# Kernel tuning notes

Hardware: AMD Instinct MI355X
Metric: run time of the kernel (lower is better)

## Reference

```python
import jax, jax.numpy as jnp
import numpy as np

N_NODES = 50000
N_EDGES = 800000
IN_FEATS = 512
NUM_HEADS = 4
OUT_FEATS = 64
NEG_SLOPE = 0.2


def setup_inputs() -> dict:
    key = jax.random.key(0)
    k1, k2, k3, k4, k5, k6 = jax.random.split(key, 6)
    feat = jax.random.normal(k1, (N_NODES, IN_FEATS), dtype=jnp.float32)
    W = jax.random.normal(k2, (IN_FEATS, NUM_HEADS * OUT_FEATS), dtype=jnp.float32) * (1.0 / np.sqrt(IN_FEATS))
    attn_l = jax.random.normal(k3, (NUM_HEADS, OUT_FEATS), dtype=jnp.float32) * (1.0 / np.sqrt(OUT_FEATS))
    attn_r = jax.random.normal(k4, (NUM_HEADS, OUT_FEATS), dtype=jnp.float32) * (1.0 / np.sqrt(OUT_FEATS))
    src = jax.random.randint(k5, (N_EDGES,), 0, N_NODES, dtype=jnp.int32)
    dst = jax.random.randint(k6, (N_EDGES,), 0, N_NODES, dtype=jnp.int32)
    return {"feat": feat, "W": W, "attn_l": attn_l, "attn_r": attn_r, "src": src, "dst": dst}


def reference(feat, W, attn_l, attn_r, src, dst):
    N = feat.shape[0]
    H, D = attn_l.shape
    # node-wise projection: fc(feat).view(N, H, D)
    ft = (feat @ W).reshape(N, H, D)
    # per-node attention logits
    el = jnp.einsum('nhd,hd->nh', ft, attn_l)  # [N, H]
    er = jnp.einsum('nhd,hd->nh', ft, attn_r)  # [N, H]
    # edge-wise score: leaky_relu(el[u] + er[v])
    e = jax.nn.leaky_relu(el[src] + er[dst], negative_slope=NEG_SLOPE)  # [E, H]
    # segment softmax over incoming edges of each destination node
    e_max = jax.ops.segment_max(e, dst, num_segments=N)  # [N, H]
    e_max = jnp.where(jnp.isfinite(e_max), e_max, 0.0)
    exp_e = jnp.exp(e - e_max[dst])  # [E, H]
    denom = jax.ops.segment_sum(exp_e, dst, num_segments=N)  # [N, H]
    a = exp_e / denom[dst]  # [E, H]
    # weighted message aggregation: sum_u a(u,v) * ft[u]
    msg = ft[src] * a[:, :, None]  # [E, H, D]
    out = jax.ops.segment_sum(msg, dst, num_segments=N)  # [N, H, D]
    return out.reshape(N, H * D)
```

## Files before the change

kernel.cpp:

```cpp
#include <hip/hip_runtime.h>

#define N_NODES 50000
#define N_EDGES 800000
#define IN_F    512
#define NH      4
#define DH      64
#define HD      256
#define NEG     0.2f
#define NB      ((N_NODES + 255) / 256)

typedef __attribute__((ext_vector_type(8))) short bf16x8;
typedef __attribute__((ext_vector_type(4))) float f32x4;

__device__ __forceinline__ unsigned short f2bf(float x) {
    unsigned u = __float_as_uint(x);
    unsigned r = (u + 0x7FFFu + ((u >> 16) & 1u)) >> 16;
    return (unsigned short)r;
}
__device__ __forceinline__ float bf2f(unsigned short b) {
    return __uint_as_float((unsigned)b << 16);
}

__global__ void zero_kernel(int* __restrict__ p, int n) {
    int i = blockIdx.x * blockDim.x + threadIdx.x;
    if (i < n) p[i] = 0;
}

__global__ __launch_bounds__(256) void count_kernel(const int* __restrict__ dst,
                                                    int* __restrict__ counts) {
    int e = blockIdx.x * blockDim.x + threadIdx.x;
    if (e < N_EDGES) atomicAdd(&counts[dst[e]], 1);
}

__global__ __launch_bounds__(256) void wt_kernel(const float* __restrict__ W,
                                                 unsigned short* __restrict__ Wtb) {
    int i = blockIdx.x * blockDim.x + threadIdx.x;
    if (i >= IN_F * HD) return;
    int k = i >> 8;
    int n = i & 255;
    Wtb[(size_t)n * IN_F + k] = f2bf(W[i]);
}

#define LDPA 72
#define LDPB 72
__global__ __launch_bounds__(256) void gemm_kernel(const float* __restrict__ A,
                                                   const unsigned short* __restrict__ Wtb,
                                                   unsigned short* __restrict__ Cb) {
    __shared__ short A_s[64][LDPA];
    __shared__ short B_s[128][LDPB];

    const int tid  = threadIdx.x;
    const int lane = tid & 63;
    const int wave = tid >> 6;
    const int wr   = wave >> 1;
    const int wc   = wave & 1;
    const int lm   = lane & 15;
    const int quad = lane >> 4;
    const int row0 = blockIdx.x * 64;
    const int col0 = blockIdx.y * 128;

    const int srow = tid >> 3;
    const int sc8  = (tid & 7) * 8;

    f32x4 acc[2][4] = {};
    float4 pa[4];
    bf16x8 pb[4];

#define LOAD_TILES(KT)                                                         \
    {                                                                          \
        int g0 = row0 + srow;                                                  \
        if (g0 < N_NODES) {                                                    \
            const float* ap = A + (size_t)g0 * IN_F + (KT) + sc8;              \
            pa[0] = *(const float4*)ap; pa[1] = *(const float4*)(ap + 4);      \
        } else { pa[0] = pa[1] = make_float4(0.f, 0.f, 0.f, 0.f); }            \
        int g1 = row0 + 32 + srow;                                             \
        if (g1 < N_NODES) {                                                    \
            const float* ap = A + (size_t)g1 * IN_F + (KT) + sc8;              \
            pa[2] = *(const float4*)ap; pa[3] = *(const float4*)(ap + 4);      \
        } else { pa[2] = pa[3] = make_float4(0.f, 0.f, 0.f, 0.f); }            \
        _Pragma("unroll")                                                      \
        for (int it = 0; it < 4; it++) {                                       \
            int brow = it * 32 + srow;                                         \
            pb[it] = *(const bf16x8*)(Wtb + (size_t)(col0 + brow) * IN_F +     \
                                      (KT) + sc8);                             \
        }                                                                      \
    }

    LOAD_TILES(0);

    for (int kt = 0; kt < IN_F; kt += 64) {
        {
            bf16x8 s;
            s[0] = (short)f2bf(pa[0].x); s[1] = (short)f2bf(pa[0].y);
            s[2] = (short)f2bf(pa[0].z); s[3] = (short)f2bf(pa[0].w);
            s[4] = (short)f2bf(pa[1].x); s[5] = (short)f2bf(pa[1].y);
            s[6] = (short)f2bf(pa[1].z); s[7] = (short)f2bf(pa[1].w);
            *(bf16x8*)(&A_s[srow][sc8]) = s;
            s[0] = (short)f2bf(pa[2].x); s[1] = (short)f2bf(pa[2].y);
            s[2] = (short)f2bf(pa[2].z); s[3] = (short)f2bf(pa[2].w);
            s[4] = (short)f2bf(pa[3].x); s[5] = (short)f2bf(pa[3].y);
            s[6] = (short)f2bf(pa[3].z); s[7] = (short)f2bf(pa[3].w);
            *(bf16x8*)(&A_s[32 + srow][sc8]) = s;
#pragma unroll
            for (int it = 0; it < 4; it++)
                *(bf16x8*)(&B_s[it * 32 + srow][sc8]) = pb[it];
        }
        __syncthreads();

        if (kt + 64 < IN_F) LOAD_TILES(kt + 64);

#pragma unroll
        for (int kk = 0; kk < 64; kk += 32) {
            bf16x8 af[2], bfr[4];
#pragma unroll
            for (int i = 0; i < 2; i++)
                af[i] = *(const bf16x8*)(&A_s[wr * 32 + i * 16 + lm][kk + quad * 8]);
#pragma unroll
            for (int j = 0; j < 4; j++)
                bfr[j] = *(const bf16x8*)(&B_s[wc * 64 + j * 16 + lm][kk + quad * 8]);
#pragma unroll
            for (int i = 0; i < 2; i++)
#pragma unroll
                for (int j = 0; j < 4; j++)
                    acc[i][j] = __builtin_amdgcn_mfma_f32_16x16x32_bf16(
                        af[i], bfr[j], acc[i][j], 0, 0, 0);
        }
        __syncthreads();
    }
#undef LOAD_TILES

#pragma unroll
    for (int i = 0; i < 2; i++) {
#pragma unroll
        for (int j = 0; j < 4; j++) {
            int gcol = col0 + wc * 64 + j * 16 + lm;
#pragma unroll
            for (int r = 0; r < 4; r++) {
                int grow = row0 + wr * 32 + i * 16 + quad * 4 + r;
                if (grow < N_NODES)
                    Cb[(size_t)grow * HD + gcol] = f2bf(acc[i][j][r]);
            }
        }
    }
}

__global__ __launch_bounds__(256) void el_er_kernel(const unsigned short* __restrict__ ftb,
                                                    const float* __restrict__ attn_l,
                                                    const float* __restrict__ attn_r,
                                                    float* __restrict__ el,
                                                    float* __restrict__ er) {
    int n    = (blockIdx.x * blockDim.x + threadIdx.x) >> 6;
    int lane = threadIdx.x & 63;
    if (n >= N_NODES) return;
    int h = lane >> 4;
    int c = lane * 4;

    ushort4 fv = *(const ushort4*)(ftb + (size_t)n * HD + c);
    float4 al = *(const float4*)(attn_l + c);
    float4 ar = *(const float4*)(attn_r + c);
    float f0 = bf2f(fv.x), f1 = bf2f(fv.y), f2 = bf2f(fv.z), f3 = bf2f(fv.w);
    float pl = f0 * al.x + f1 * al.y + f2 * al.z + f3 * al.w;
    float pr = f0 * ar.x + f1 * ar.y + f2 * ar.z + f3 * ar.w;
#pragma unroll
    for (int off = 8; off > 0; off >>= 1) {
        pl += __shfl_down(pl, off);
        pr += __shfl_down(pr, off);
    }
    if ((lane & 15) == 0) {
        el[(size_t)n * NH + h] = pl;
        er[(size_t)n * NH + h] = pr;
    }
}

__global__ __launch_bounds__(256) void partial_kernel(const int* __restrict__ counts,
                                                      int* __restrict__ bsums) {
    __shared__ int red[4];
    int i = blockIdx.x * 256 + threadIdx.x;
    int c = (i < N_NODES) ? counts[i] : 0;
#pragma unroll
    for (int off = 32; off > 0; off >>= 1) c += __shfl_down(c, off);
    if ((threadIdx.x & 63) == 0) red[threadIdx.x >> 6] = c;
    __syncthreads();
    if (threadIdx.x == 0) bsums[blockIdx.x] = red[0] + red[1] + red[2] + red[3];
}

__global__ __launch_bounds__(256) void bscan_kernel(const int* __restrict__ bsums,
                                                    int* __restrict__ boffs) {
    __shared__ int s[256];
    int tid = threadIdx.x;
    s[tid] = (tid < NB) ? bsums[tid] : 0;
    __syncthreads();
    for (int off = 1; off < 256; off <<= 1) {
        int x = s[tid];
        int a = (tid >= off) ? s[tid - off] : 0;
        __syncthreads();
        s[tid] = x + a;
        __syncthreads();
    }
    if (tid < NB) boffs[tid] = (tid > 0) ? s[tid - 1] : 0;
}

__global__ __launch_bounds__(256) void scatter_scan_kernel(const int* __restrict__ counts,
                                                           const int* __restrict__ boffs,
                                                           int* __restrict__ offsets,
                                                           int* __restrict__ cursor) {
    __shared__ int s[256];
    int tid = threadIdx.x;
    int i = blockIdx.x * 256 + tid;
    s[tid] = (i < N_NODES) ? counts[i] : 0;
    __syncthreads();
    for (int off = 1; off < 256; off <<= 1) {
        int x = s[tid];
        int a = (tid >= off) ? s[tid - off] : 0;
        __syncthreads();
        s[tid] = x + a;
        __syncthreads();
    }
    int excl = (tid > 0) ? s[tid - 1] : 0;
    int o = boffs[blockIdx.x] + excl;
    if (i < N_NODES) { offsets[i] = o; cursor[i] = o; }
    if (i == 0) offsets[N_NODES] = N_EDGES;
}

__device__ __forceinline__ float lrelu_exp(float x) {
    float y = (x > 0.f) ? x : NEG * x;
    return __expf(y);
}

__global__ __launch_bounds__(256) void edge_place_kernel(const int* __restrict__ src,
                                                         const int* __restrict__ dst,
                                                         const float* __restrict__ el,
                                                         const float* __restrict__ er,
                                                         int* __restrict__ cursor,
                                                         int* __restrict__ srcs,
                                                         float* __restrict__ w4s) {
    int e = blockIdx.x * blockDim.x + threadIdx.x;
    if (e >= N_EDGES) return;
    int u = src[e], v = dst[e];
    float4 l = *(const float4*)(el + (size_t)u * NH);
    float4 r = *(const float4*)(er + (size_t)v * NH);
    float4 s;
    s.x = lrelu_exp(l.x + r.x);
    s.y = lrelu_exp(l.y + r.y);
    s.z = lrelu_exp(l.z + r.z);
    s.w = lrelu_exp(l.w + r.w);
    int pos = atomicAdd(&cursor[v], 1);
    srcs[pos] = u;
    *(float4*)(w4s + (size_t)pos * NH) = s;
}

__global__ __launch_bounds__(256) void agg_kernel(const unsigned short* __restrict__ ftb,
                                                  const float* __restrict__ w4s,
                                                  const int* __restrict__ srcs,
                                                  const int* __restrict__ offsets,
                                                  float* __restrict__ out) {
    int wv   = (blockIdx.x * blockDim.x + threadIdx.x) >> 6;
    int lane = threadIdx.x & 63;
    if (wv >= N_NODES) return;

    const int beg = offsets[wv];
    const int end = offsets[wv + 1];
    const int h   = lane >> 4;
    const size_t foff = (size_t)lane * 4;

    float4 acc = make_float4(0.f, 0.f, 0.f, 0.f);
    float dsum = 0.f;

    const int n4 = (end - beg) >> 2;
    int u0, u1, u2, u3;
    if (n4 > 0) {
        const int* sp = srcs + beg;
        u0 = sp[0]; u1 = sp[1]; u2 = sp[2]; u3 = sp[3];
        for (int b = 0; b < n4; b++) {
            const int base = beg + b * 4;
            int v0 = 0, v1 = 0, v2 = 0, v3 = 0;
            if (b + 1 < n4) {
                const int* np = srcs + base + 4;
                v0 = np[0]; v1 = np[1]; v2 = np[2]; v3 = np[3];
            }
            ushort4 f0 = *(const ushort4*)(ftb + (size_t)u0 * HD + foff);
            ushort4 f1 = *(const ushort4*)(ftb + (size_t)u1 * HD + foff);
            ushort4 f2 = *(const ushort4*)(ftb + (size_t)u2 * HD + foff);
            ushort4 f3 = *(const ushort4*)(ftb + (size_t)u3 * HD + foff);
            float w0 = w4s[(size_t)(base + 0) * NH + h];
            float w1 = w4s[(size_t)(base + 1) * NH + h];
            float w2 = w4s[(size_t)(base + 2) * NH + h];
            float w3 = w4s[(size_t)(base + 3) * NH + h];
            acc.x += w0 * bf2f(f0.x) + w1 * bf2f(f1.x) + w2 * bf2f(f2.x) + w3 * bf2f(f3.x);
            acc.y += w0 * bf2f(f0.y) + w1 * bf2f(f1.y) + w2 * bf2f(f2.y) + w3 * bf2f(f3.y);
            acc.z += w0 * bf2f(f0.z) + w1 * bf2f(f1.z) + w2 * bf2f(f2.z) + w3 * bf2f(f3.z);
            acc.w += w0 * bf2f(f0.w) + w1 * bf2f(f1.w) + w2 * bf2f(f2.w) + w3 * bf2f(f3.w);
            dsum += (w0 + w1) + (w2 + w3);
            u0 = v0; u1 = v1; u2 = v2; u3 = v3;
        }
    }
    for (int p = beg + n4 * 4; p < end; p++) {
        int u = srcs[p];
        float w = w4s[(size_t)p * NH + h];
        ushort4 f = *(const ushort4*)(ftb + (size_t)u * HD + foff);
        acc.x += w * bf2f(f.x);
        acc.y += w * bf2f(f.y);
        acc.z += w * bf2f(f.z);
        acc.w += w * bf2f(f.w);
        dsum += w;
    }

    float inv = (dsum > 0.f) ? (1.f / dsum) : 0.f;
    acc.x *= inv; acc.y *= inv; acc.z *= inv; acc.w *= inv;
    *(float4*)(out + (size_t)wv * HD + foff) = acc;
}

extern "C" void kernel_launch(void* const* d_in, const int* in_sizes, int n_in,
                              void* d_out, int out_size, void* d_ws, size_t ws_size,
                              hipStream_t stream) {
    const float* feat   = (const float*)d_in[0];
    const float* W      = (const float*)d_in[1];
    const float* attn_l = (const float*)d_in[2];
    const float* attn_r = (const float*)d_in[3];
    const int*   src    = (const int*)d_in[4];
    const int*   dst    = (const int*)d_in[5];
    float* out = (float*)d_out;

    char* p = (char*)d_ws;
    auto alloc = [&](size_t bytes) -> char* {
        char* r = p;
        p += (bytes + 255) & ~(size_t)255;
        return r;
    };
    unsigned short* ftb     = (unsigned short*)alloc((size_t)N_NODES * HD * 2);
    unsigned short* Wtb     = (unsigned short*)alloc((size_t)IN_F * HD * 2);
    float*          el      = (float*)alloc((size_t)N_NODES * NH * 4);
    float*          er      = (float*)alloc((size_t)N_NODES * NH * 4);
    float*          w4s     = (float*)alloc((size_t)N_EDGES * NH * 4);
    int*            srcs    = (int*)alloc((size_t)N_EDGES * 4);
    int*            counts  = (int*)alloc((size_t)N_NODES * 4);
    int*            offsets = (int*)alloc((size_t)(N_NODES + 1) * 4);
    int*            cursor  = (int*)alloc((size_t)N_NODES * 4);
    int*            bsums   = (int*)alloc((size_t)NB * 4);
    int*            boffs   = (int*)alloc((size_t)NB * 4);

    zero_kernel<<<(N_NODES + 255) / 256, 256, 0, stream>>>(counts, N_NODES);
    count_kernel<<<(N_EDGES + 255) / 256, 256, 0, stream>>>(dst, counts);
    wt_kernel<<<(IN_F * HD + 255) / 256, 256, 0, stream>>>(W, Wtb);
    dim3 ggrid((N_NODES + 63) / 64, HD / 128);
    gemm_kernel<<<ggrid, 256, 0, stream>>>(feat, Wtb, ftb);
    el_er_kernel<<<(N_NODES + 3) / 4, 256, 0, stream>>>(ftb, attn_l, attn_r, el, er);
    partial_kernel<<<NB, 256, 0, stream>>>(counts, bsums);
    bscan_kernel<<<1, 256, 0, stream>>>(bsums, boffs);
    scatter_scan_kernel<<<NB, 256, 0, stream>>>(counts, boffs, offsets, cursor);
    edge_place_kernel<<<(N_EDGES + 255) / 256, 256, 0, stream>>>(src, dst, el, er,
                                                                 cursor, srcs, w4s);
    agg_kernel<<<(N_NODES + 3) / 4, 256, 0, stream>>>(ftb, w4s, srcs, offsets, out);
}
```

Before: 350.7 us.

## Fuse attention logits into full-width GEMM epilogue and merge setup kernels

The GEMM now computes all 256 output columns per block, with each wave owning one head, so feat rows are read once instead of twice. The per-node el/er dot products are computed from the fp32 accumulators in the epilogue using cross-lane shuffles, which removes the separate el_er kernel and its re-read of ft. Zeroing the counts and transposing W are merged into one launch. In exchange, each block holds more accumulators and twice the B tile in LDS, so occupancy may drop, and there are half as many GEMM blocks.

After: 345.0 us. No clear change (-1.6%).

```diff
diff --git a/kernel.cpp b/kernel.cpp
--- a/kernel.cpp
+++ b/kernel.cpp
@@ -21,9 +21,21 @@
     return __uint_as_float((unsigned)b << 16);
 }
 
-__global__ void zero_kernel(int* __restrict__ p, int n) {
-    int i = blockIdx.x * blockDim.x + threadIdx.x;
-    if (i < n) p[i] = 0;
+__global__ __launch_bounds__(256) void setup_kernel(const float* __restrict__ W,
+                                                    unsigned short* __restrict__ Wtb,
+                                                    int* __restrict__ counts) {
+    int b = blockIdx.x;
+    if (b < NB) {
+        int i = b * 256 + threadIdx.x;
+        if (i < N_NODES) counts[i] = 0;
+    } else {
+        int i = (b - NB) * 256 + threadIdx.x;
+        if (i < IN_F * HD) {
+            int k = i >> 8;
+            int n = i & 255;
+            Wtb[(size_t)n * IN_F + k] = f2bf(W[i]);
+        }
+    }
 }
 
 __global__ __launch_bounds__(256) void count_kernel(const int* __restrict__ dst,
@@ -32,39 +44,31 @@
     if (e < N_EDGES) atomicAdd(&counts[dst[e]], 1);
 }
 
-__global__ __launch_bounds__(256) void wt_kernel(const float* __restrict__ W,
-                                                 unsigned short* __restrict__ Wtb) {
-    int i = blockIdx.x * blockDim.x + threadIdx.x;
-    if (i >= IN_F * HD) return;
-    int k = i >> 8;
-    int n = i & 255;
-    Wtb[(size_t)n * IN_F + k] = f2bf(W[i]);
-}
-
 #define LDPA 72
 #define LDPB 72
 __global__ __launch_bounds__(256) void gemm_kernel(const float* __restrict__ A,
                                                    const unsigned short* __restrict__ Wtb,
-                                                   unsigned short* __restrict__ Cb) {
+                                                   const float* __restrict__ attn_l,
+                                                   const float* __restrict__ attn_r,
+                                                   unsigned short* __restrict__ Cb,
+                                                   float* __restrict__ el,
+                                                   float* __restrict__ er) {
     __shared__ short A_s[64][LDPA];
-    __shared__ short B_s[128][LDPB];
+    __shared__ short B_s[256][LDPB];
 
     const int tid  = threadIdx.x;
     const int lane = tid & 63;
-    const int wave = tid >> 6;
-    const int wr   = wave >> 1;
-    const int wc   = wave & 1;
+    const int w    = tid >> 6;
     const int lm   = lane & 15;
     const int quad = lane >> 4;
     const int row0 = blockIdx.x * 64;
-    const int col0 = blockIdx.y * 128;
 
     const int srow = tid >> 3;
     const int sc8  = (tid & 7) * 8;
 
-    f32x4 acc[2][4] = {};
+    f32x4 acc[4][4] = {};
     float4 pa[4];
-    bf16x8 pb[4];
+    bf16x8 pb[8];
 
 #define LOAD_TILES(KT)                                                         \
     {                                                                          \
@@ -79,9 +83,9 @@
             pa[2] = *(const float4*)ap; pa[3] = *(const float4*)(ap + 4);      \
         } else { pa[2] = pa[3] = make_float4(0.f, 0.f, 0.f, 0.f); }            \
         _Pragma("unroll")                                                      \
-        for (int it = 0; it < 4; it++) {                                       \
+        for (int it = 0; it < 8; it++) {                                       \
             int brow = it * 32 + srow;                                         \
-            pb[it] = *(const bf16x8*)(Wtb + (size_t)(col0 + brow) * IN_F +     \
+            pb[it] = *(const bf16x8*)(Wtb + (size_t)brow * IN_F +              \
                                       (KT) + sc8);                             \
         }                                                                      \
     }
@@ -102,7 +106,7 @@
             s[6] = (short)f2bf(pa[3].z); s[7] = (short)f2bf(pa[3].w);
             *(bf16x8*)(&A_s[32 + srow][sc8]) = s;
 #pragma unroll
-            for (int it = 0; it < 4; it++)
+            for (int it = 0; it < 8; it++)
                 *(bf16x8*)(&B_s[it * 32 + srow][sc8]) = pb[it];
         }
         __syncthreads();
@@ -111,15 +115,15 @@
 
 #pragma unroll
         for (int kk = 0; kk < 64; kk += 32) {
-            bf16x8 af[2], bfr[4];
-#pragma unroll
-            for (int i = 0; i < 2; i++)
-                af[i] = *(const bf16x8*)(&A_s[wr * 32 + i * 16 + lm][kk + quad * 8]);
+            bf16x8 af[4], bfr[4];
+#pragma unroll
+            for (int i = 0; i < 4; i++)
+                af[i] = *(const bf16x8*)(&A_s[i * 16 + lm][kk + quad * 8]);
 #pragma unroll
             for (int j = 0; j < 4; j++)
-                bfr[j] = *(const bf16x8*)(&B_s[wc * 64 + j * 16 + lm][kk + quad * 8]);
-#pragma unroll
-            for (int i = 0; i < 2; i++)
+                bfr[j] = *(const bf16x8*)(&B_s[w * 64 + j * 16 + lm][kk + quad * 8]);
+#pragma unroll
+            for (int i = 0; i < 4; i++)
 #pragma unroll
                 for (int j = 0; j < 4; j++)
                     acc[i][j] = __builtin_amdgcn_mfma_f32_16x16x32_bf16(
@@ -130,45 +134,50 @@
 #undef LOAD_TILES
 
 #pragma unroll
-    for (int i = 0; i < 2; i++) {
+    for (int i = 0; i < 4; i++) {
 #pragma unroll
         for (int j = 0; j < 4; j++) {
-            int gcol = col0 + wc * 64 + j * 16 + lm;
+            int gcol = w * 64 + j * 16 + lm;
 #pragma unroll
             for (int r = 0; r < 4; r++) {
-                int grow = row0 + wr * 32 + i * 16 + quad * 4 + r;
+                int grow = row0 + i * 16 + quad * 4 + r;
                 if (grow < N_NODES)
                     Cb[(size_t)grow * HD + gcol] = f2bf(acc[i][j][r]);
             }
         }
     }
-}
-
-__global__ __launch_bounds__(256) void el_er_kernel(const unsigned short* __restrict__ ftb,
-                                                    const float* __restrict__ attn_l,
-                                                    const float* __restrict__ attn_r,
-                                                    float* __restrict__ el,
-                                                    float* __restrict__ er) {
-    int n    = (blockIdx.x * blockDim.x + threadIdx.x) >> 6;
-    int lane = threadIdx.x & 63;
-    if (n >= N_NODES) return;
-    int h = lane >> 4;
-    int c = lane * 4;
-
-    ushort4 fv = *(const ushort4*)(ftb + (size_t)n * HD + c);
-    float4 al = *(const float4*)(attn_l + c);
-    float4 ar = *(const float4*)(attn_r + c);
-    float f0 = bf2f(fv.x), f1 = bf2f(fv.y), f2 = bf2f(fv.z), f3 = bf2f(fv.w);
-    float pl = f0 * al.x + f1 * al.y + f2 * al.z + f3 * al.w;
-    float pr = f0 * ar.x + f1 * ar.y + f2 * ar.z + f3 * ar.w;
-#pragma unroll
-    for (int off = 8; off > 0; off >>= 1) {
-        pl += __shfl_down(pl, off);
-        pr += __shfl_down(pr, off);
-    }
-    if ((lane & 15) == 0) {
-        el[(size_t)n * NH + h] = pl;
-        er[(size_t)n * NH + h] = pr;
+
+    {
+        float al[4], ar[4];
+#pragma unroll
+        for (int j = 0; j < 4; j++) {
+            al[j] = attn_l[w * DH + j * 16 + lm];
+            ar[j] = attn_r[w * DH + j * 16 + lm];
+        }
+#pragma unroll
+        for (int i = 0; i < 4; i++) {
+#pragma unroll
+            for (int r = 0; r < 4; r++) {
+                float sl = 0.f, sr = 0.f;
+#pragma unroll
+                for (int j = 0; j < 4; j++) {
+                    sl += acc[i][j][r] * al[j];
+                    sr += acc[i][j][r] * ar[j];
+                }
+#pragma unroll
+                for (int off = 8; off > 0; off >>= 1) {
+                    sl += __shfl_xor(sl, off);
+                    sr += __shfl_xor(sr, off);
+                }
+                if (lm == 0) {
+                    int grow = row0 + i * 16 + quad * 4 + r;
+                    if (grow < N_NODES) {
+                        el[(size_t)grow * NH + w] = sl;
+                        er[(size_t)grow * NH + w] = sr;
+                    }
+                }
+            }
+        }
     }
 }
 
@@ -339,12 +348,10 @@
     int*            bsums   = (int*)alloc((size_t)NB * 4);
     int*            boffs   = (int*)alloc((size_t)NB * 4);
 
-    zero_kernel<<<(N_NODES + 255) / 256, 256, 0, stream>>>(counts, N_NODES);
+    setup_kernel<<<NB + (IN_F * HD + 255) / 256, 256, 0, stream>>>(W, Wtb, counts);
     count_kernel<<<(N_EDGES + 255) / 256, 256, 0, stream>>>(dst, counts);
-    wt_kernel<<<(IN_F * HD + 255) / 256, 256, 0, stream>>>(W, Wtb);
-    dim3 ggrid((N_NODES + 63) / 64, HD / 128);
-    gemm_kernel<<<ggrid, 256, 0, stream>>>(feat, Wtb, ftb);
-    el_er_kernel<<<(N_NODES + 3) / 4, 256, 0, stream>>>(ftb, attn_l, attn_r, el, er);
+    gemm_kernel<<<(N_NODES + 63) / 64, 256, 0, stream>>>(feat, Wtb, attn_l, attn_r,
+                                                         ftb, el, er);
     partial_kernel<<<NB, 256, 0, stream>>>(counts, bsums);
     bscan_kernel<<<1, 256, 0, stream>>>(bsums, boffs);
     scatter_scan_kernel<<<NB, 256, 0, stream>>>(counts, boffs, offsets, cursor);
```
